# Kernel optimization log

Hardware: AMD Instinct MI355X
Metric: run time of the kernel (lower is better)

Reference implementation:

```python
import jax, jax.numpy as jnp
import numpy as np

B, JX, JM, D, H = 8, 2048, 2048, 512, 512
NEG_INF = -1e30


def setup_inputs() -> dict:
    key = jax.random.key(0)
    ks = jax.random.split(key, 6)
    inputs = jax.random.normal(ks[0], (B, JX, D), dtype=jnp.float32)
    memory = jax.random.normal(ks[1], (B, JM, D), dtype=jnp.float32)
    mask = jax.random.randint(ks[2], (B, JM), 0, 2, dtype=jnp.int32)
    # guarantee at least one valid memory slot per row
    mask = mask.at[:, 0].set(1)
    Wq = jax.random.normal(ks[3], (D, H), dtype=jnp.float32) * 0.05
    Wk = jax.random.normal(ks[4], (D, H), dtype=jnp.float32) * 0.05
    Wg = jax.random.normal(ks[5], (2 * D, 2 * D), dtype=jnp.float32) * 0.05
    return {"inputs": inputs, "memory": memory, "mask": mask,
            "Wq": Wq, "Wk": Wk, "Wg": Wg}


def reference(inputs, memory, mask, Wq, Wk, Wg):
    hidden = Wq.shape[-1]
    # two ReLU projections (no bias)
    q = jax.nn.relu(jnp.einsum('bxd,dh->bxh', inputs, Wq))   # [B,JX,H]
    k = jax.nn.relu(jnp.einsum('bmd,dh->bmh', memory, Wk))   # [B,JM,H]
    # scaled dot-product scores
    scores = jnp.einsum('bxh,bmh->bxm', q, k) / (hidden ** 0.5)  # [B,JX,JM]
    # softmax_mask: -inf where mask == 0 (broadcast over JX instead of tile)
    m = mask[:, None, :].astype(scores.dtype)                 # [B,1,JM]
    scores = scores * m + (1.0 - m) * NEG_INF
    logits = jax.nn.softmax(scores, axis=-1)                  # [B,JX,JM]
    # attend over RAW memory (not projected)
    att = jnp.einsum('bxm,bmd->bxd', logits, memory)          # [B,JX,D]
    # gate combiner: concat -> dense(sigmoid, no bias) -> multiply
    res = jnp.concatenate([inputs, att], axis=-1)             # [B,JX,2D]
    g = jax.nn.sigmoid(jnp.einsum('bxe,ef->bxf', res, Wg))
    return res * g
```

## Files before the change

### kernel.cpp

```cpp
#include <hip/hip_runtime.h>

typedef unsigned short u16;
typedef unsigned int   u32;

typedef short s16x8 __attribute__((ext_vector_type(8)));
typedef float f32x4 __attribute__((ext_vector_type(4)));

static __device__ __forceinline__ u16 f2bf(float f) {
  u32 u = __float_as_uint(f);
  u = (u + 0x7fffu + ((u >> 16) & 1u)) >> 16;
  return (u16)u;
}
static __device__ __forceinline__ float bf2f(u16 h) {
  return __uint_as_float(((u32)h) << 16);
}
static __device__ __forceinline__ f32x4 mfma16(s16x8 a, s16x8 b, f32x4 c) {
  return __builtin_amdgcn_mfma_f32_16x16x32_bf16(a, b, c, 0, 0, 0);
}
static __device__ __forceinline__ void gload16(const u16* g, u16* l) {
  __builtin_amdgcn_global_load_lds(
      (const __attribute__((address_space(1))) void*)g,
      (__attribute__((address_space(3))) void*)l, 16, 0, 0);
}

#define WAITVM8() asm volatile("s_waitcnt vmcnt(8)" ::: "memory")
#define WAITVM0() asm volatile("s_waitcnt vmcnt(0)" ::: "memory")
#define BAR()                                  \
  do {                                         \
    asm volatile("" ::: "memory");             \
    __builtin_amdgcn_s_barrier();              \
    asm volatile("" ::: "memory");             \
  } while (0)

__global__ __launch_bounds__(256) void cvt_k(const float* __restrict__ in,
                                             u16* __restrict__ out, int n8) {
  int i = blockIdx.x * 256 + threadIdx.x;
  if (i >= n8) return;
  const float4* p = reinterpret_cast<const float4*>(in);
  float4 a = p[2 * i], b = p[2 * i + 1];
  union { u16 u[8]; uint4 v; } r;
  r.u[0] = f2bf(a.x); r.u[1] = f2bf(a.y); r.u[2] = f2bf(a.z); r.u[3] = f2bf(a.w);
  r.u[4] = f2bf(b.x); r.u[5] = f2bf(b.y); r.u[6] = f2bf(b.z); r.u[7] = f2bf(b.w);
  reinterpret_cast<uint4*>(out)[i] = r.v;
}

__global__ void tcvt_k(const float* __restrict__ in, u16* __restrict__ out,
                       int R, int C, long long ibs, long long obs) {
  __shared__ float t[32][33];
  const float* ip = in + (size_t)blockIdx.z * ibs;
  u16* op = out + (size_t)blockIdx.z * obs;
  int r0 = blockIdx.y * 32, c0 = blockIdx.x * 32;
  int x = threadIdx.x, y = threadIdx.y;
  for (int i = y; i < 32; i += 8) t[i][x] = ip[(size_t)(r0 + i) * C + c0 + x];
  __syncthreads();
  for (int i = y; i < 32; i += 8) op[(size_t)(c0 + i) * R + r0 + x] = f2bf(t[x][i]);
}

__global__ __launch_bounds__(256) void softmax_k(u16* __restrict__ P,
                                                 const int* __restrict__ mask,
                                                 float scale) {
  __shared__ float redm[4], reds[4];
  const int row = blockIdx.x;
  const int bb = row >> 11;
  const int tid = threadIdx.x;
  u16* p = P + (size_t)row * 2048;
  const int* mk = mask + (size_t)bb * 2048;
  uint4 raw = reinterpret_cast<const uint4*>(p)[tid];
  int4 ma = reinterpret_cast<const int4*>(mk)[2 * tid];
  int4 mc = reinterpret_cast<const int4*>(mk)[2 * tid + 1];
  float v[8];
  v[0] = ma.x ? bf2f((u16)(raw.x & 0xffff)) * scale : -1e30f;
  v[1] = ma.y ? bf2f((u16)(raw.x >> 16))    * scale : -1e30f;
  v[2] = ma.z ? bf2f((u16)(raw.y & 0xffff)) * scale : -1e30f;
  v[3] = ma.w ? bf2f((u16)(raw.y >> 16))    * scale : -1e30f;
  v[4] = mc.x ? bf2f((u16)(raw.z & 0xffff)) * scale : -1e30f;
  v[5] = mc.y ? bf2f((u16)(raw.z >> 16))    * scale : -1e30f;
  v[6] = mc.z ? bf2f((u16)(raw.w & 0xffff)) * scale : -1e30f;
  v[7] = mc.w ? bf2f((u16)(raw.w >> 16))    * scale : -1e30f;
  float mx = v[0];
  #pragma unroll
  for (int i = 1; i < 8; ++i) mx = fmaxf(mx, v[i]);
  for (int off = 32; off; off >>= 1) mx = fmaxf(mx, __shfl_xor(mx, off));
  if ((tid & 63) == 0) redm[tid >> 6] = mx;
  __syncthreads();
  mx = fmaxf(fmaxf(redm[0], redm[1]), fmaxf(redm[2], redm[3]));
  float sum = 0.f;
  #pragma unroll
  for (int i = 0; i < 8; ++i) { v[i] = __expf(v[i] - mx); sum += v[i]; }
  for (int off = 32; off; off >>= 1) sum += __shfl_xor(sum, off);
  if ((tid & 63) == 0) reds[tid >> 6] = sum;
  __syncthreads();
  sum = reds[0] + reds[1] + reds[2] + reds[3];
  float inv = 1.0f / sum;
  union { u16 u[8]; uint4 q; } r;
  #pragma unroll
  for (int i = 0; i < 8; ++i) r.u[i] = f2bf(v[i] * inv);
  reinterpret_cast<uint4*>(p)[tid] = r.q;
}

template <int EPI, int NT, int NX, int NY,
          int LDA, int LDB, int LDC, int KSPLIT, int MSPLIT,
          long long ABS, long long BBS, long long CBS, int NWG>
__global__ __launch_bounds__(256, 2) void gdb(
    const u16* __restrict__ A, const u16* __restrict__ A2,
    const u16* __restrict__ Bt, const u16* __restrict__ Bt2,
    float* __restrict__ Cf, u16* __restrict__ Cb,
    const float* __restrict__ R0, const u16* __restrict__ R1) {
  __shared__ u16 As[2][128 * 64];
  __shared__ u16 Bs[2][128 * 64];
  const int bid = blockIdx.x;
  const int wgid = (bid & 7) * (NWG / 8) + (bid >> 3);
  const int bx = wgid % NX;
  const int by = (wgid / NX) % NY;
  const int bz = wgid / (NX * NY);
  const int tid = threadIdx.x;
  const int wave = tid >> 6, lane = tid & 63;
  const int m0 = by * 128, n0 = bx * 128;
  const int wr = wave >> 1, wc = wave & 1;
  const int l15 = lane & 15, l4 = lane >> 4;
  const int srow = lane >> 3;
  const int scolsw = (((lane & 7) ^ (lane >> 3)) << 3);
  const int rsw = (l15 & 7) << 3;
  const u16* Bbase = ((m0 < MSPLIT) ? Bt : Bt2) + (size_t)bz * BBS;
  const u16* Abase0 = A + (size_t)bz * ABS;
  const u16* Abase1 = A2 + (size_t)bz * ABS;

  f32x4 acc[4][4];
  #pragma unroll
  for (int i = 0; i < 4; ++i)
    #pragma unroll
    for (int j = 0; j < 4; ++j) acc[i][j] = (f32x4){0.f, 0.f, 0.f, 0.f};

  auto stage = [&](int buf, int k0) {
    const u16* Ab;
    int kl;
    if (k0 < KSPLIT) { Ab = Abase0; kl = k0; }
    else             { Ab = Abase1; kl = k0 - KSPLIT; }
    #pragma unroll
    for (int c = 0; c < 4; ++c) {
      int chunk = wave * 4 + c;
      int row = chunk * 8 + srow;
      gload16(Ab + (size_t)(m0 + row) * LDA + kl + scolsw, &As[buf][chunk * 512]);
      gload16(Bbase + (size_t)(n0 + row) * LDB + k0 + scolsw, &Bs[buf][chunk * 512]);
    }
  };
  auto compute = [&](int cur) {
    __builtin_amdgcn_s_setprio(1);
    #pragma unroll
    for (int kk = 0; kk < 64; kk += 32) {
      s16x8 af[4], bfr[4];
      #pragma unroll
      for (int mi = 0; mi < 4; ++mi)
        af[mi] = *reinterpret_cast<const s16x8*>(
            &As[cur][(wr * 64 + mi * 16 + l15) * 64 + ((kk + l4 * 8) ^ rsw)]);
      #pragma unroll
      for (int ni = 0; ni < 4; ++ni)
        bfr[ni] = *reinterpret_cast<const s16x8*>(
            &Bs[cur][(wc * 64 + ni * 16 + l15) * 64 + ((kk + l4 * 8) ^ rsw)]);
      #pragma unroll
      for (int mi = 0; mi < 4; ++mi)
        #pragma unroll
        for (int ni = 0; ni < 4; ++ni)
          acc[mi][ni] = mfma16(af[mi], bfr[ni], acc[mi][ni]);
    }
    __builtin_amdgcn_s_setprio(0);
  };

  stage(0, 0);
  stage(1, 64);
  WAITVM8();
  BAR();
  for (int t = 0; t < NT; ++t) {
    const int cur = t & 1;
    compute(cur);
    BAR();
    if (t + 2 < NT) stage(cur, (t + 2) * 64);
    if (t + 1 < NT) {
      if (t + 2 < NT) { WAITVM8(); } else { WAITVM0(); }
      BAR();
    }
  }

  float* LF = (float*)(&As[0][0]);
  const int er = tid >> 3;
  const int ec = (tid & 7) * 16;
  #pragma unroll
  for (int mi = 0; mi < 4; ++mi) {
    __syncthreads();
    #pragma unroll
    for (int ni = 0; ni < 4; ++ni) {
      int lcol = wc * 64 + ni * 16 + l15;
      #pragma unroll
      for (int j = 0; j < 4; ++j)
        LF[(wr * 16 + l4 * 4 + j) * 132 + lcol] = acc[mi][ni][j];
    }
    __syncthreads();
    int grow = m0 + mi * 16 + (er & 15) + (er >> 4) * 64;
    int gcol = n0 + ec;
    float v[16];
    #pragma unroll
    for (int i = 0; i < 4; ++i)
      *reinterpret_cast<f32x4*>(&v[4 * i]) =
          *reinterpret_cast<const f32x4*>(&LF[er * 132 + ec + 4 * i]);
    if (EPI == 3) {
      float* o = Cf + (size_t)bz * CBS + (size_t)grow * LDC + gcol;
      if (n0 < 512) {
        const float* r0 = R0 + (size_t)grow * 512 + gcol;
        #pragma unroll
        for (int i = 0; i < 16; ++i) {
          float g = 1.0f / (1.0f + __expf(-v[i]));
          v[i] = r0[i] * g;
        }
      } else {
        const u16* r1 = R1 + (size_t)grow * 512 + (gcol - 512);
        #pragma unroll
        for (int i = 0; i < 16; ++i) {
          float g = 1.0f / (1.0f + __expf(-v[i]));
          v[i] = bf2f(r1[i]) * g;
        }
      }
      #pragma unroll
      for (int i = 0; i < 4; ++i)
        *reinterpret_cast<float4*>(&o[4 * i]) = *reinterpret_cast<float4*>(&v[4 * i]);
    } else {
      union { u16 u[16]; uint4 q[2]; } pk;
      #pragma unroll
      for (int i = 0; i < 16; ++i)
        pk.u[i] = f2bf(EPI == 0 ? fmaxf(v[i], 0.f) : v[i]);
      u16* o = Cb + (size_t)bz * CBS + (size_t)grow * LDC + gcol;
      reinterpret_cast<uint4*>(o)[0] = pk.q[0];
      reinterpret_cast<uint4*>(o)[1] = pk.q[1];
    }
  }
}

extern "C" void kernel_launch(void* const* d_in, const int* in_sizes, int n_in,
                              void* d_out, int out_size, void* d_ws, size_t ws_size,
                              hipStream_t stream) {
  const float* inputs = (const float*)d_in[0];
  const float* memory = (const float*)d_in[1];
  const int*   mask   = (const int*)d_in[2];
  const float* Wq     = (const float*)d_in[3];
  const float* Wk     = (const float*)d_in[4];
  const float* Wg     = (const float*)d_in[5];
  float* out = (float*)d_out;

  char* ws = (char*)d_ws;
  size_t off = 0;
  auto alloc = [&](size_t bytes) {
    void* p = ws + off;
    off += (bytes + 255) & ~(size_t)255;
    return p;
  };
  u16* in_b  = (u16*)alloc(16384ULL * 512 * 2);
  u16* mem_b = (u16*)alloc(16384ULL * 512 * 2);
  u16* memT  = (u16*)alloc(16384ULL * 512 * 2);
  u16* WqT   = (u16*)alloc(512ULL * 512 * 2);
  u16* WkT   = (u16*)alloc(512ULL * 512 * 2);
  u16* WgT   = (u16*)alloc(1024ULL * 1024 * 2);
  u16* q_b   = (u16*)alloc(16384ULL * 512 * 2);
  u16* k_b   = (u16*)alloc(16384ULL * 512 * 2);
  u16* sc    = (u16*)alloc(8ULL * 2048 * 2048 * 2);
  u16* att_b = (u16*)alloc(16384ULL * 512 * 2);
  (void)ws_size; (void)in_sizes; (void)n_in; (void)out_size; (void)mem_b;

  const int n8 = (16384 * 512) / 8;
  cvt_k<<<(n8 + 255) / 256, 256, 0, stream>>>(inputs, in_b, n8);
  cvt_k<<<(n8 + 255) / 256, 256, 0, stream>>>(memory, in_b + 16384ULL * 512, n8);
  dim3 tb(32, 8);
  tcvt_k<<<dim3(16, 16, 1), tb, 0, stream>>>(Wq, WqT, 512, 512, 0, 0);
  tcvt_k<<<dim3(16, 16, 1), tb, 0, stream>>>(Wk, WkT, 512, 512, 0, 0);
  tcvt_k<<<dim3(32, 32, 1), tb, 0, stream>>>(Wg, WgT, 1024, 1024, 0, 0);
  tcvt_k<<<dim3(16, 64, 8), tb, 0, stream>>>(memory, memT, 2048, 512,
                                             2048LL * 512, 2048LL * 512);

  const int BIG = 1 << 30;

  gdb<0, 8, 4, 256, 512, 512, 512, (1 << 30), 16384, 0, 0, 0, 1024>
      <<<1024, 256, 0, stream>>>(in_b, in_b, WqT, WkT, nullptr, q_b,
                                 nullptr, nullptr);

  gdb<1, 8, 16, 16, 512, 512, 2048, (1 << 30), (1 << 30),
      2048LL * 512, 2048LL * 512, 2048LL * 2048, 2048>
      <<<2048, 256, 0, stream>>>(q_b, q_b, k_b, k_b, nullptr, sc,
                                 nullptr, nullptr);

  softmax_k<<<16384, 256, 0, stream>>>(sc, mask, 0.044194173824159216f);

  gdb<1, 32, 4, 16, 2048, 2048, 512, (1 << 30), (1 << 30),
      2048LL * 2048, 512LL * 2048, 2048LL * 512, 512>
      <<<512, 256, 0, stream>>>(sc, sc, memT, memT, nullptr, att_b,
                                nullptr, nullptr);

  gdb<3, 16, 8, 128, 512, 1024, 1024, 512, (1 << 30), 0, 0, 0, 1024>
      <<<1024, 256, 0, stream>>>(in_b, att_b, WgT, WgT, out, nullptr,
                                 inputs, att_b);
  (void)BIG;
}
```

Measured before the change: 235.5 us.

## Add 256x256-tile 8-wave GEMM kernel for projection, score and gate GEMMs

Introduces a new GEMM kernel with 256x256 output tiles, 512 threads (8 waves), double-buffered 128KB LDS, and loads for the next K-step interleaved between quarter-step MFMA phases with s_setprio. It replaces the 128x128 kernel for the Q/K projections, the QK^T score GEMM and the gated output GEMM, while the attention GEMM stays on the old kernel, whose sigmoid-gate epilogue is removed. Larger tiles halve operand reloads per output and raise arithmetic intensity. The cost is fewer workgroups (256 or 512 across 256 CUs), heavier LDS use that limits occupancy to one block per CU, and many barriers per K-step.

```diff
diff --git a/kernel.cpp b/kernel.cpp
--- a/kernel.cpp
+++ b/kernel.cpp
@@ -24,6 +24,8 @@
 }
 
 #define WAITVM8() asm volatile("s_waitcnt vmcnt(8)" ::: "memory")
+#define WAITVM4() asm volatile("s_waitcnt vmcnt(4)" ::: "memory")
+#define WAITVM2() asm volatile("s_waitcnt vmcnt(2)" ::: "memory")
 #define WAITVM0() asm volatile("s_waitcnt vmcnt(0)" ::: "memory")
 #define BAR()                                  \
   do {                                         \
@@ -96,6 +98,190 @@
   #pragma unroll
   for (int i = 0; i < 8; ++i) r.u[i] = f2bf(v[i] * inv);
   reinterpret_cast<uint4*>(p)[tid] = r.q;
+}
+
+template <int EPI, int NT, int NX, int NY, int LDA, int LDB, int LDC,
+          int KSPLIT, int MSPLIT, long long ABS, long long BBS, long long CBS,
+          int NWG>
+__global__ __launch_bounds__(512) void g256(
+    const u16* __restrict__ A, const u16* __restrict__ A2,
+    const u16* __restrict__ Bt, const u16* __restrict__ Bt2,
+    float* __restrict__ Cf, u16* __restrict__ Cb,
+    const float* __restrict__ R0, const u16* __restrict__ R1) {
+  __shared__ u16 SM[65536];
+  const int bid = blockIdx.x;
+  const int wgid = (bid & 7) * (NWG / 8) + (bid >> 3);
+  const int bx = wgid % NX;
+  const int by = (wgid / NX) % NY;
+  const int bz = wgid / (NX * NY);
+  const int tid = threadIdx.x;
+  const int wave = tid >> 6, lane = tid & 63;
+  const int m0 = by * 256, n0 = bx * 256;
+  const int wr = wave >> 2, wc = wave & 3;
+  const int l15 = lane & 15, l4 = lane >> 4;
+  const int scolsw = (((tid & 7) ^ ((tid >> 3) & 7)) << 3);
+  const u16* Bbase = ((m0 < MSPLIT) ? Bt : Bt2) + (size_t)bz * BBS;
+  const u16* Ab0 = A + (size_t)bz * ABS;
+  const u16* Ab1 = A2 + (size_t)bz * ABS;
+
+  f32x4 acc[8][4];
+  #pragma unroll
+  for (int i = 0; i < 8; ++i)
+    #pragma unroll
+    for (int j = 0; j < 4; ++j) acc[i][j] = (f32x4){0.f, 0.f, 0.f, 0.f};
+
+  auto ASb = [&](int buf) -> u16* { return SM + buf * 16384; };
+  auto BSb = [&](int buf) -> u16* { return SM + 32768 + buf * 16384; };
+
+  auto stA = [&](int buf, int k0, int r) {
+    const u16* Ab; int kl;
+    if (k0 < KSPLIT) { Ab = Ab0; kl = k0; } else { Ab = Ab1; kl = k0 - KSPLIT; }
+    gload16(Ab + (size_t)(m0 + r * 64 + (tid >> 3)) * LDA + kl + scolsw,
+            ASb(buf) + r * 4096 + tid * 8);
+  };
+  auto stB = [&](int buf, int k0, int r) {
+    gload16(Bbase + (size_t)(n0 + r * 64 + (tid >> 3)) * LDB + k0 + scolsw,
+            BSb(buf) + r * 4096 + tid * 8);
+  };
+  auto ldf = [&](const u16* base, int row, int kq) {
+    int slot = (kq * 4 + l4) ^ (row & 7);
+    return *reinterpret_cast<const s16x8*>(base + row * 64 + slot * 8);
+  };
+
+  #pragma unroll
+  for (int r = 0; r < 4; ++r) stB(0, 0, r);
+  #pragma unroll
+  for (int r = 0; r < 4; ++r) stA(0, 0, r);
+  WAITVM0();
+  BAR();
+
+  for (int t = 0; t < NT; ++t) {
+    const int c = t & 1;
+    const int nk = (t + 1) * 64;
+    const bool st = (t + 1 < NT);
+    s16x8 bfr[4][2], af[4];
+
+    #pragma unroll
+    for (int ni = 0; ni < 4; ++ni)
+      #pragma unroll
+      for (int kq = 0; kq < 2; ++kq)
+        bfr[ni][kq] = ldf(BSb(c), wc * 64 + ni * 16 + l15, kq);
+    #pragma unroll
+    for (int mi = 0; mi < 4; ++mi)
+      af[mi] = ldf(ASb(c), wr * 128 + mi * 16 + l15, 0);
+    if (st) { stB(c ^ 1, nk, 0); stB(c ^ 1, nk, 1); }
+    BAR();
+    __builtin_amdgcn_s_setprio(1);
+    #pragma unroll
+    for (int mi = 0; mi < 4; ++mi)
+      #pragma unroll
+      for (int ni = 0; ni < 4; ++ni)
+        acc[mi][ni] = mfma16(af[mi], bfr[ni][0], acc[mi][ni]);
+    __builtin_amdgcn_s_setprio(0);
+    BAR();
+
+    #pragma unroll
+    for (int mi = 0; mi < 4; ++mi)
+      af[mi] = ldf(ASb(c), wr * 128 + mi * 16 + l15, 1);
+    if (st) { stB(c ^ 1, nk, 2); stB(c ^ 1, nk, 3); }
+    BAR();
+    __builtin_amdgcn_s_setprio(1);
+    #pragma unroll
+    for (int mi = 0; mi < 4; ++mi)
+      #pragma unroll
+      for (int ni = 0; ni < 4; ++ni)
+        acc[mi][ni] = mfma16(af[mi], bfr[ni][1], acc[mi][ni]);
+    __builtin_amdgcn_s_setprio(0);
+    if (st) { WAITVM4(); } else { WAITVM0(); }
+    BAR();
+
+    #pragma unroll
+    for (int mi = 0; mi < 4; ++mi)
+      af[mi] = ldf(ASb(c), wr * 128 + 64 + mi * 16 + l15, 0);
+    if (st) { stA(c ^ 1, nk, 0); stA(c ^ 1, nk, 2); }
+    BAR();
+    __builtin_amdgcn_s_setprio(1);
+    #pragma unroll
+    for (int mi = 0; mi < 4; ++mi)
+      #pragma unroll
+      for (int ni = 0; ni < 4; ++ni)
+        acc[4 + mi][ni] = mfma16(af[mi], bfr[ni][0], acc[4 + mi][ni]);
+    __builtin_amdgcn_s_setprio(0);
+    BAR();
+
+    #pragma unroll
+    for (int mi = 0; mi < 4; ++mi)
+      af[mi] = ldf(ASb(c), wr * 128 + 64 + mi * 16 + l15, 1);
+    if (st) { stA(c ^ 1, nk, 1); stA(c ^ 1, nk, 3); }
+    BAR();
+    __builtin_amdgcn_s_setprio(1);
+    #pragma unroll
+    for (int mi = 0; mi < 4; ++mi)
+      #pragma unroll
+      for (int ni = 0; ni < 4; ++ni)
+        acc[4 + mi][ni] = mfma16(af[mi], bfr[ni][1], acc[4 + mi][ni]);
+    __builtin_amdgcn_s_setprio(0);
+    if (st) { WAITVM2(); } else { WAITVM0(); }
+    BAR();
+  }
+
+  float* LF = (float*)SM;
+  #pragma unroll
+  for (int ci = 0; ci < 4; ++ci) {
+    __syncthreads();
+    #pragma unroll
+    for (int u = 0; u < 2; ++u) {
+      #pragma unroll
+      for (int ni = 0; ni < 4; ++ni) {
+        int lr = wr * 32 + u * 16 + l4 * 4;
+        int lc = wc * 64 + ni * 16 + l15;
+        #pragma unroll
+        for (int j = 0; j < 4; ++j)
+          LF[(lr + j) * 260 + lc] = acc[2 * ci + u][ni][j];
+      }
+    }
+    __syncthreads();
+    int r = tid >> 3;
+    int cb = (tid & 7) * 32;
+    int b = r >> 5, sub = r & 31;
+    int mf = 2 * ci + (sub >> 4);
+    int grow = m0 + b * 128 + (mf >> 2) * 64 + (mf & 3) * 16 + (sub & 15);
+    int gcol = n0 + cb;
+    float v[32];
+    #pragma unroll
+    for (int i = 0; i < 8; ++i)
+      *reinterpret_cast<f32x4*>(&v[4 * i]) =
+          *reinterpret_cast<const f32x4*>(&LF[r * 260 + cb + 4 * i]);
+    if (EPI == 3) {
+      float* o = Cf + (size_t)bz * CBS + (size_t)grow * LDC + gcol;
+      if (n0 < 512) {
+        const float* r0 = R0 + (size_t)grow * 512 + gcol;
+        #pragma unroll
+        for (int i = 0; i < 32; ++i) {
+          float g = 1.0f / (1.0f + __expf(-v[i]));
+          v[i] = r0[i] * g;
+        }
+      } else {
+        const u16* r1 = R1 + (size_t)grow * 512 + (gcol - 512);
+        #pragma unroll
+        for (int i = 0; i < 32; ++i) {
+          float g = 1.0f / (1.0f + __expf(-v[i]));
+          v[i] = bf2f(r1[i]) * g;
+        }
+      }
+      #pragma unroll
+      for (int i = 0; i < 8; ++i)
+        reinterpret_cast<float4*>(o)[i] = *reinterpret_cast<float4*>(&v[4 * i]);
+    } else {
+      union { u16 u[32]; uint4 q[4]; } pk;
+      #pragma unroll
+      for (int i = 0; i < 32; ++i)
+        pk.u[i] = f2bf(EPI == 0 ? fmaxf(v[i], 0.f) : v[i]);
+      u16* o = Cb + (size_t)bz * CBS + (size_t)grow * LDC + gcol;
+      #pragma unroll
+      for (int i = 0; i < 4; ++i) reinterpret_cast<uint4*>(o)[i] = pk.q[i];
+    }
+  }
 }
 
 template <int EPI, int NT, int NX, int NY,
@@ -202,36 +388,15 @@
     for (int i = 0; i < 4; ++i)
       *reinterpret_cast<f32x4*>(&v[4 * i]) =
           *reinterpret_cast<const f32x4*>(&LF[er * 132 + ec + 4 * i]);
-    if (EPI == 3) {
-      float* o = Cf + (size_t)bz * CBS + (size_t)grow * LDC + gcol;
-      if (n0 < 512) {
-        const float* r0 = R0 + (size_t)grow * 512 + gcol;
-        #pragma unroll
-        for (int i = 0; i < 16; ++i) {
-          float g = 1.0f / (1.0f + __expf(-v[i]));
-          v[i] = r0[i] * g;
-        }
-      } else {
-        const u16* r1 = R1 + (size_t)grow * 512 + (gcol - 512);
-        #pragma unroll
-        for (int i = 0; i < 16; ++i) {
-          float g = 1.0f / (1.0f + __expf(-v[i]));
-          v[i] = bf2f(r1[i]) * g;
-        }
-      }
-      #pragma unroll
-      for (int i = 0; i < 4; ++i)
-        *reinterpret_cast<float4*>(&o[4 * i]) = *reinterpret_cast<float4*>(&v[4 * i]);
-    } else {
-      union { u16 u[16]; uint4 q[2]; } pk;
-      #pragma unroll
-      for (int i = 0; i < 16; ++i)
-        pk.u[i] = f2bf(EPI == 0 ? fmaxf(v[i], 0.f) : v[i]);
-      u16* o = Cb + (size_t)bz * CBS + (size_t)grow * LDC + gcol;
-      reinterpret_cast<uint4*>(o)[0] = pk.q[0];
-      reinterpret_cast<uint4*>(o)[1] = pk.q[1];
-    }
+    union { u16 u[16]; uint4 q[2]; } pk;
+    #pragma unroll
+    for (int i = 0; i < 16; ++i)
+      pk.u[i] = f2bf(EPI == 0 ? fmaxf(v[i], 0.f) : v[i]);
+    u16* o = Cb + (size_t)bz * CBS + (size_t)grow * LDC + gcol;
+    reinterpret_cast<uint4*>(o)[0] = pk.q[0];
+    reinterpret_cast<uint4*>(o)[1] = pk.q[1];
   }
+  (void)Cf; (void)R0; (void)R1;
 }
 
 extern "C" void kernel_launch(void* const* d_in, const int* in_sizes, int n_in,
@@ -274,16 +439,14 @@
   tcvt_k<<<dim3(16, 64, 8), tb, 0, stream>>>(memory, memT, 2048, 512,
                                              2048LL * 512, 2048LL * 512);
 
-  const int BIG = 1 << 30;
-
-  gdb<0, 8, 4, 256, 512, 512, 512, (1 << 30), 16384, 0, 0, 0, 1024>
-      <<<1024, 256, 0, stream>>>(in_b, in_b, WqT, WkT, nullptr, q_b,
-                                 nullptr, nullptr);
-
-  gdb<1, 8, 16, 16, 512, 512, 2048, (1 << 30), (1 << 30),
-      2048LL * 512, 2048LL * 512, 2048LL * 2048, 2048>
-      <<<2048, 256, 0, stream>>>(q_b, q_b, k_b, k_b, nullptr, sc,
-                                 nullptr, nullptr);
+  g256<0, 8, 2, 128, 512, 512, 512, (1 << 30), 16384, 0, 0, 0, 256>
+      <<<256, 512, 0, stream>>>(in_b, in_b, WqT, WkT, nullptr, q_b,
+                                nullptr, nullptr);
+
+  g256<1, 8, 8, 8, 512, 512, 2048, (1 << 30), (1 << 30),
+       2048LL * 512, 2048LL * 512, 2048LL * 2048, 512>
+      <<<512, 512, 0, stream>>>(q_b, q_b, k_b, k_b, nullptr, sc,
+                                nullptr, nullptr);
 
   softmax_k<<<16384, 256, 0, stream>>>(sc, mask, 0.044194173824159216f);
 
@@ -292,8 +455,7 @@
       <<<512, 256, 0, stream>>>(sc, sc, memT, memT, nullptr, att_b,
                                 nullptr, nullptr);
 
-  gdb<3, 16, 8, 128, 512, 1024, 1024, 512, (1 << 30), 0, 0, 0, 1024>
-      <<<1024, 256, 0, stream>>>(in_b, att_b, WgT, WgT, out, nullptr,
-                                 inputs, att_b);
-  (void)BIG;
-}
+  g256<3, 16, 4, 64, 512, 1024, 1024, 512, (1 << 30), 0, 0, 0, 256>
+      <<<256, 512, 0, stream>>>(in_b, att_b, WgT, WgT, out, nullptr,
+                                inputs, att_b);
+}
```

After: 246.7 us. +4.7%, slower.

## Add 128x64-tile GEMM variant and fuse memory convert with transpose

Applied to the files above, without the earlier changes.

Adds a gdb64 GEMM kernel with a 128x64 output tile, a smaller B shared buffer and launch bounds allowing three blocks per CU. The projection, score and gate GEMMs switch to it, doubling their grid sizes. The aim is better occupancy and less tail imbalance, at the cost of less data reuse per block. Separately, the two memory conversion kernels (row-major bf16 and transposed bf16) are merged into one cvtT_k pass so memory is read once. The old gdb epilogue drops its unused EPI==3 path.

```diff
diff --git a/kernel.cpp b/kernel.cpp
--- a/kernel.cpp
+++ b/kernel.cpp
@@ -24,6 +24,7 @@
 }
 
 #define WAITVM8() asm volatile("s_waitcnt vmcnt(8)" ::: "memory")
+#define WAITVM6() asm volatile("s_waitcnt vmcnt(6)" ::: "memory")
 #define WAITVM0() asm volatile("s_waitcnt vmcnt(0)" ::: "memory")
 #define BAR()                                  \
   do {                                         \
@@ -42,6 +43,21 @@
   r.u[0] = f2bf(a.x); r.u[1] = f2bf(a.y); r.u[2] = f2bf(a.z); r.u[3] = f2bf(a.w);
   r.u[4] = f2bf(b.x); r.u[5] = f2bf(b.y); r.u[6] = f2bf(b.z); r.u[7] = f2bf(b.w);
   reinterpret_cast<uint4*>(out)[i] = r.v;
+}
+
+__global__ void cvtT_k(const float* __restrict__ in, u16* __restrict__ rm,
+                       u16* __restrict__ tr) {
+  __shared__ float t[32][33];
+  const int z = blockIdx.z;
+  const float* ip = in + (size_t)z * 2048 * 512;
+  int r0 = blockIdx.y * 32, c0 = blockIdx.x * 32;
+  int x = threadIdx.x, y = threadIdx.y;
+  for (int i = y; i < 32; i += 8) t[i][x] = ip[(size_t)(r0 + i) * 512 + c0 + x];
+  __syncthreads();
+  u16* rp = rm + (size_t)z * 2048 * 512;
+  u16* tp = tr + (size_t)z * 512 * 2048;
+  for (int i = y; i < 32; i += 8) rp[(size_t)(r0 + i) * 512 + c0 + x] = f2bf(t[i][x]);
+  for (int i = y; i < 32; i += 8) tp[(size_t)(c0 + i) * 2048 + r0 + x] = f2bf(t[x][i]);
 }
 
 __global__ void tcvt_k(const float* __restrict__ in, u16* __restrict__ out,
@@ -96,6 +112,145 @@
   #pragma unroll
   for (int i = 0; i < 8; ++i) r.u[i] = f2bf(v[i] * inv);
   reinterpret_cast<uint4*>(p)[tid] = r.q;
+}
+
+template <int EPI, int NT, int NX, int NY,
+          int LDA, int LDB, int LDC, int KSPLIT, int MSPLIT,
+          long long ABS, long long BBS, long long CBS, int NWG>
+__global__ __launch_bounds__(256, 3) void gdb64(
+    const u16* __restrict__ A, const u16* __restrict__ A2,
+    const u16* __restrict__ Bt, const u16* __restrict__ Bt2,
+    float* __restrict__ Cf, u16* __restrict__ Cb,
+    const float* __restrict__ R0, const u16* __restrict__ R1) {
+  __shared__ u16 As[2][128 * 64];
+  __shared__ u16 Bs[2][64 * 64];
+  const int bid = blockIdx.x;
+  const int wgid = (bid & 7) * (NWG / 8) + (bid >> 3);
+  const int bx = wgid % NX;
+  const int by = (wgid / NX) % NY;
+  const int bz = wgid / (NX * NY);
+  const int tid = threadIdx.x;
+  const int wave = tid >> 6, lane = tid & 63;
+  const int m0 = by * 128, n0 = bx * 64;
+  const int wr = wave >> 1, wc = wave & 1;
+  const int l15 = lane & 15, l4 = lane >> 4;
+  const int srow = lane >> 3;
+  const int scolsw = (((lane & 7) ^ (lane >> 3)) << 3);
+  const int rsw = (l15 & 7) << 3;
+  const u16* Bbase = ((m0 < MSPLIT) ? Bt : Bt2) + (size_t)bz * BBS;
+  const u16* Abase0 = A + (size_t)bz * ABS;
+  const u16* Abase1 = A2 + (size_t)bz * ABS;
+
+  f32x4 acc[4][2];
+  #pragma unroll
+  for (int i = 0; i < 4; ++i)
+    #pragma unroll
+    for (int j = 0; j < 2; ++j) acc[i][j] = (f32x4){0.f, 0.f, 0.f, 0.f};
+
+  auto stage = [&](int buf, int k0) {
+    const u16* Ab;
+    int kl;
+    if (k0 < KSPLIT) { Ab = Abase0; kl = k0; }
+    else             { Ab = Abase1; kl = k0 - KSPLIT; }
+    #pragma unroll
+    for (int c = 0; c < 4; ++c) {
+      int chunk = wave * 4 + c;
+      int row = chunk * 8 + srow;
+      gload16(Ab + (size_t)(m0 + row) * LDA + kl + scolsw, &As[buf][chunk * 512]);
+    }
+    #pragma unroll
+    for (int c = 0; c < 2; ++c) {
+      int chunk = wave * 2 + c;
+      int row = chunk * 8 + srow;
+      gload16(Bbase + (size_t)(n0 + row) * LDB + k0 + scolsw, &Bs[buf][chunk * 512]);
+    }
+  };
+  auto compute = [&](int cur) {
+    __builtin_amdgcn_s_setprio(1);
+    #pragma unroll
+    for (int kk = 0; kk < 64; kk += 32) {
+      s16x8 af[4], bfr[2];
+      #pragma unroll
+      for (int mi = 0; mi < 4; ++mi)
+        af[mi] = *reinterpret_cast<const s16x8*>(
+            &As[cur][(wr * 64 + mi * 16 + l15) * 64 + ((kk + l4 * 8) ^ rsw)]);
+      #pragma unroll
+      for (int ni = 0; ni < 2; ++ni)
+        bfr[ni] = *reinterpret_cast<const s16x8*>(
+            &Bs[cur][(wc * 32 + ni * 16 + l15) * 64 + ((kk + l4 * 8) ^ rsw)]);
+      #pragma unroll
+      for (int mi = 0; mi < 4; ++mi)
+        #pragma unroll
+        for (int ni = 0; ni < 2; ++ni)
+          acc[mi][ni] = mfma16(af[mi], bfr[ni], acc[mi][ni]);
+    }
+    __builtin_amdgcn_s_setprio(0);
+  };
+
+  stage(0, 0);
+  stage(1, 64);
+  WAITVM6();
+  BAR();
+  for (int t = 0; t < NT; ++t) {
+    const int cur = t & 1;
+    compute(cur);
+    BAR();
+    if (t + 2 < NT) stage(cur, (t + 2) * 64);
+    if (t + 1 < NT) {
+      if (t + 2 < NT) { WAITVM6(); } else { WAITVM0(); }
+      BAR();
+    }
+  }
+
+  float* LF = (float*)(&As[0][0]);
+  const int er = tid >> 3;
+  const int ec = (tid & 7) * 8;
+  #pragma unroll
+  for (int mi = 0; mi < 4; ++mi) {
+    __syncthreads();
+    #pragma unroll
+    for (int ni = 0; ni < 2; ++ni) {
+      int lc = wc * 32 + ni * 16 + l15;
+      #pragma unroll
+      for (int j = 0; j < 4; ++j)
+        LF[(wr * 16 + l4 * 4 + j) * 68 + lc] = acc[mi][ni][j];
+    }
+    __syncthreads();
+    int grow = m0 + (er >> 4) * 64 + mi * 16 + (er & 15);
+    int gcol = n0 + ec;
+    float v[8];
+    #pragma unroll
+    for (int i = 0; i < 2; ++i)
+      *reinterpret_cast<f32x4*>(&v[4 * i]) =
+          *reinterpret_cast<const f32x4*>(&LF[er * 68 + ec + 4 * i]);
+    if (EPI == 3) {
+      float* o = Cf + (size_t)bz * CBS + (size_t)grow * LDC + gcol;
+      if (n0 < 512) {
+        const float* r0 = R0 + (size_t)grow * 512 + gcol;
+        #pragma unroll
+        for (int i = 0; i < 8; ++i) {
+          float g = 1.0f / (1.0f + __expf(-v[i]));
+          v[i] = r0[i] * g;
+        }
+      } else {
+        const u16* r1 = R1 + (size_t)grow * 512 + (gcol - 512);
+        #pragma unroll
+        for (int i = 0; i < 8; ++i) {
+          float g = 1.0f / (1.0f + __expf(-v[i]));
+          v[i] = bf2f(r1[i]) * g;
+        }
+      }
+      reinterpret_cast<float4*>(o)[0] = *reinterpret_cast<float4*>(&v[0]);
+      reinterpret_cast<float4*>(o)[1] = *reinterpret_cast<float4*>(&v[4]);
+    } else {
+      union { u16 u[8]; uint4 q; } pk;
+      #pragma unroll
+      for (int i = 0; i < 8; ++i)
+        pk.u[i] = f2bf(EPI == 0 ? fmaxf(v[i], 0.f) : v[i]);
+      u16* o = Cb + (size_t)bz * CBS + (size_t)grow * LDC + gcol;
+      reinterpret_cast<uint4*>(o)[0] = pk.q;
+    }
+  }
 }
 
 template <int EPI, int NT, int NX, int NY,
@@ -202,36 +357,15 @@
     for (int i = 0; i < 4; ++i)
       *reinterpret_cast<f32x4*>(&v[4 * i]) =
           *reinterpret_cast<const f32x4*>(&LF[er * 132 + ec + 4 * i]);
-    if (EPI == 3) {
-      float* o = Cf + (size_t)bz * CBS + (size_t)grow * LDC + gcol;
-      if (n0 < 512) {
-        const float* r0 = R0 + (size_t)grow * 512 + gcol;
-        #pragma unroll
-        for (int i = 0; i < 16; ++i) {
-          float g = 1.0f / (1.0f + __expf(-v[i]));
-          v[i] = r0[i] * g;
-        }
-      } else {
-        const u16* r1 = R1 + (size_t)grow * 512 + (gcol - 512);
-        #pragma unroll
-        for (int i = 0; i < 16; ++i) {
-          float g = 1.0f / (1.0f + __expf(-v[i]));
-          v[i] = bf2f(r1[i]) * g;
-        }
-      }
-      #pragma unroll
-      for (int i = 0; i < 4; ++i)
-        *reinterpret_cast<float4*>(&o[4 * i]) = *reinterpret_cast<float4*>(&v[4 * i]);
-    } else {
-      union { u16 u[16]; uint4 q[2]; } pk;
-      #pragma unroll
-      for (int i = 0; i < 16; ++i)
-        pk.u[i] = f2bf(EPI == 0 ? fmaxf(v[i], 0.f) : v[i]);
-      u16* o = Cb + (size_t)bz * CBS + (size_t)grow * LDC + gcol;
-      reinterpret_cast<uint4*>(o)[0] = pk.q[0];
-      reinterpret_cast<uint4*>(o)[1] = pk.q[1];
-    }
+    union { u16 u[16]; uint4 q[2]; } pk;
+    #pragma unroll
+    for (int i = 0; i < 16; ++i)
+      pk.u[i] = f2bf(EPI == 0 ? fmaxf(v[i], 0.f) : v[i]);
+    u16* o = Cb + (size_t)bz * CBS + (size_t)grow * LDC + gcol;
+    reinterpret_cast<uint4*>(o)[0] = pk.q[0];
+    reinterpret_cast<uint4*>(o)[1] = pk.q[1];
   }
+  (void)Cf; (void)R0; (void)R1;
 }
 
 extern "C" void kernel_launch(void* const* d_in, const int* in_sizes, int n_in,
@@ -262,27 +396,26 @@
   u16* k_b   = (u16*)alloc(16384ULL * 512 * 2);
   u16* sc    = (u16*)alloc(8ULL * 2048 * 2048 * 2);
   u16* att_b = (u16*)alloc(16384ULL * 512 * 2);
-  (void)ws_size; (void)in_sizes; (void)n_in; (void)out_size; (void)mem_b;
+  (void)ws_size; (void)in_sizes; (void)n_in; (void)out_size;
 
   const int n8 = (16384 * 512) / 8;
   cvt_k<<<(n8 + 255) / 256, 256, 0, stream>>>(inputs, in_b, n8);
-  cvt_k<<<(n8 + 255) / 256, 256, 0, stream>>>(memory, in_b + 16384ULL * 512, n8);
+  cvtT_k<<<dim3(16, 64, 8), dim3(32, 8), 0, stream>>>(memory, mem_b, memT);
   dim3 tb(32, 8);
   tcvt_k<<<dim3(16, 16, 1), tb, 0, stream>>>(Wq, WqT, 512, 512, 0, 0);
   tcvt_k<<<dim3(16, 16, 1), tb, 0, stream>>>(Wk, WkT, 512, 512, 0, 0);
   tcvt_k<<<dim3(32, 32, 1), tb, 0, stream>>>(Wg, WgT, 1024, 1024, 0, 0);
-  tcvt_k<<<dim3(16, 64, 8), tb, 0, stream>>>(memory, memT, 2048, 512,
-                                             2048LL * 512, 2048LL * 512);
 
   const int BIG = 1 << 30;
-
-  gdb<0, 8, 4, 256, 512, 512, 512, (1 << 30), 16384, 0, 0, 0, 1024>
-      <<<1024, 256, 0, stream>>>(in_b, in_b, WqT, WkT, nullptr, q_b,
+  (void)BIG;
+
+  gdb64<0, 8, 8, 256, 512, 512, 512, (1 << 30), 16384, 0, 0, 0, 2048>
+      <<<2048, 256, 0, stream>>>(in_b, in_b, WqT, WkT, nullptr, q_b,
                                  nullptr, nullptr);
 
-  gdb<1, 8, 16, 16, 512, 512, 2048, (1 << 30), (1 << 30),
-      2048LL * 512, 2048LL * 512, 2048LL * 2048, 2048>
-      <<<2048, 256, 0, stream>>>(q_b, q_b, k_b, k_b, nullptr, sc,
+  gdb64<1, 8, 32, 16, 512, 512, 2048, (1 << 30), (1 << 30),
+        2048LL * 512, 2048LL * 512, 2048LL * 2048, 4096>
+      <<<4096, 256, 0, stream>>>(q_b, q_b, k_b, k_b, nullptr, sc,
                                  nullptr, nullptr);
 
   softmax_k<<<16384, 256, 0, stream>>>(sc, mask, 0.044194173824159216f);
@@ -292,8 +425,7 @@
       <<<512, 256, 0, stream>>>(sc, sc, memT, memT, nullptr, att_b,
                                 nullptr, nullptr);
 
-  gdb<3, 16, 8, 128, 512, 1024, 1024, 512, (1 << 30), 0, 0, 0, 1024>
-      <<<1024, 256, 0, stream>>>(in_b, att_b, WgT, WgT, out, nullptr,
+  gdb64<3, 16, 16, 128, 512, 1024, 1024, 512, (1 << 30), 0, 0, 0, 2048>
+      <<<2048, 256, 0, stream>>>(in_b, att_b, WgT, WgT, out, nullptr,
                                  inputs, att_b);
-  (void)BIG;
-}
+}
```

After: 234.7 us. Within noise of the previous version (-0.4%).
